# Optimization experiments

Hardware: AMD Instinct MI355X
Metric: run time of the kernel (lower is better)

Reference implementation:

```python
import jax, jax.numpy as jnp
import numpy as np

F, B, D = 32, 8192, 64  # num fields, batch, embedding dim


def setup_inputs() -> dict:
    key = jax.random.key(0)
    inputs = jax.random.normal(key, (F, B, 1, D), dtype=jnp.float32)
    return {"inputs": inputs}


def reference(inputs) -> jnp.ndarray:
    # OPnnLayer with use_reduce=True, use_flatten=True.
    # 1) Add() over the field list -> [B, 1, D]
    s = jnp.sum(inputs, axis=0)  # [B, 1, D]
    # 2) InnerLayer(use_inner=False, perm=[0,2,1]): batch_dot(s^T, s)
    #    [B, D, 1] @ [B, 1, D] -> [B, D, D] (rank-1 outer product per sample)
    outer = jnp.einsum('bod,boe->bde', s, s)  # o == 1
    # 3) Flatten -> [B, D*D]
    return outer.reshape(outer.shape[0], -1)
```

## Files before the change

kernel.cpp:

```cpp
#include <hip/hip_runtime.h>


#define NF 32
#define NB 8192
#define ND 64

__global__ __launch_bounds__(256) void opnn_outer_kernel(
    const float* __restrict__ in, float* __restrict__ out) {
    const int tid = threadIdx.x;
    const int b   = blockIdx.x;
    const int g    = tid >> 4;
    const int dvec = tid & 15;

    const float4* in4 = (const float4*)in;
    size_t i0 = ((size_t)(2 * g)     * NB + b) * (ND / 4) + dvec;
    size_t i1 = ((size_t)(2 * g + 1) * NB + b) * (ND / 4) + dvec;
    float4 a0 = in4[i0];
    float4 a1 = in4[i1];
    float4 acc = make_float4(a0.x + a1.x, a0.y + a1.y, a0.z + a1.z, a0.w + a1.w);

    __shared__ float4 part[16][16];
    __shared__ float4 s4[16];
    part[g][dvec] = acc;
    __syncthreads();

    if (tid < 16) {
        float4 sum = part[0][tid];
        #pragma unroll
        for (int gg = 1; gg < 16; ++gg) {
            float4 p = part[gg][tid];
            sum.x += p.x; sum.y += p.y; sum.z += p.z; sum.w += p.w;
        }
        s4[tid] = sum;
    }
    __syncthreads();

    const float* s = (const float*)s4;
    float4* out4 = (float4*)(out + (size_t)b * (ND * ND));
    #pragma unroll
    for (int j = 0; j < 4; ++j) {
        int idx4 = j * 256 + tid;
        int r  = idx4 >> 4;
        int cv = idx4 & 15;
        float  sr = s[r];
        float4 sc = s4[cv];
        out4[idx4] = make_float4(sr * sc.x, sr * sc.y, sr * sc.z, sr * sc.w);
    }
}

extern "C" void kernel_launch(void* const* d_in, const int* in_sizes, int n_in,
                              void* d_out, int out_size, void* d_ws, size_t ws_size,
                              hipStream_t stream) {
    const float* in = (const float*)d_in[0];
    float* out = (float*)d_out;
    opnn_outer_kernel<<<NB, 256, 0, stream>>>(in, out);
}
```

Measured before the change: 181.6 us.

## Process sixteen samples per block with in-register field sum and nontemporal stores

Each block now handles 16 batch samples instead of one. Each thread sums all 32 fields for its float4 slice in registers, which removes the two-stage shared-memory reduction and one barrier. Each wavefront then writes four samples' outer products using nontemporal loads and stores to keep streaming data out of the cache. The grid shrinks to 512 blocks, which may leave the GPU's compute units less evenly occupied, and the 32 loads per thread are serialized per lane.

```diff
diff --git a/kernel.cpp b/kernel.cpp
--- a/kernel.cpp
+++ b/kernel.cpp
@@ -5,46 +5,45 @@
 #define NB 8192
 #define ND 64
 
+typedef float f4 __attribute__((ext_vector_type(4)));
+
 __global__ __launch_bounds__(256) void opnn_outer_kernel(
     const float* __restrict__ in, float* __restrict__ out) {
-    const int tid = threadIdx.x;
-    const int b   = blockIdx.x;
-    const int g    = tid >> 4;
-    const int dvec = tid & 15;
+    const int tid  = threadIdx.x;
+    const int w    = tid >> 6;
+    const int lane = tid & 63;
+    const int lb   = lane >> 4;
+    const int dv   = lane & 15;
+    const int s_local = w * 4 + lb;
+    const int b = blockIdx.x * 16 + s_local;
 
-    const float4* in4 = (const float4*)in;
-    size_t i0 = ((size_t)(2 * g)     * NB + b) * (ND / 4) + dvec;
-    size_t i1 = ((size_t)(2 * g + 1) * NB + b) * (ND / 4) + dvec;
-    float4 a0 = in4[i0];
-    float4 a1 = in4[i1];
-    float4 acc = make_float4(a0.x + a1.x, a0.y + a1.y, a0.z + a1.z, a0.w + a1.w);
+    const f4* __restrict__ in4 = (const f4*)in;
+    const size_t base = (size_t)b * (ND / 4) + dv;
+    f4 acc = (f4)0.f;
+    #pragma unroll
+    for (int f = 0; f < NF; ++f) {
+        f4 v = __builtin_nontemporal_load(&in4[base + (size_t)f * NB * (ND / 4)]);
+        acc += v;
+    }
 
-    __shared__ float4 part[16][16];
-    __shared__ float4 s4[16];
-    part[g][dvec] = acc;
+    __shared__ f4 sh[16][16];
+    sh[s_local][dv] = acc;
     __syncthreads();
 
-    if (tid < 16) {
-        float4 sum = part[0][tid];
+    const float* shf = (const float*)sh;
+    #pragma unroll
+    for (int ss = 0; ss < 4; ++ss) {
+        const int sidx = w * 4 + ss;
+        const f4 sc = sh[sidx][dv];
+        f4* __restrict__ outp =
+            (f4*)(out + ((size_t)blockIdx.x * 16 + sidx) * (ND * ND));
         #pragma unroll
-        for (int gg = 1; gg < 16; ++gg) {
-            float4 p = part[gg][tid];
-            sum.x += p.x; sum.y += p.y; sum.z += p.z; sum.w += p.w;
+        for (int it = 0; it < 16; ++it) {
+            const int r = it * 4 + lb;
+            const float sr = shf[sidx * 64 + r];
+            f4 v = sr * sc;
+            __builtin_nontemporal_store(v, &outp[it * 64 + lane]);
         }
-        s4[tid] = sum;
-    }
-    __syncthreads();
-
-    const float* s = (const float*)s4;
-    float4* out4 = (float4*)(out + (size_t)b * (ND * ND));
-    #pragma unroll
-    for (int j = 0; j < 4; ++j) {
-        int idx4 = j * 256 + tid;
-        int r  = idx4 >> 4;
-        int cv = idx4 & 15;
-        float  sr = s[r];
-        float4 sc = s4[cv];
-        out4[idx4] = make_float4(sr * sc.x, sr * sc.y, sr * sc.z, sr * sc.w);
     }
 }
 
@@ -53,5 +52,5 @@
                               hipStream_t stream) {
     const float* in = (const float*)d_in[0];
     float* out = (float*)d_out;
-    opnn_outer_kernel<<<NB, 256, 0, stream>>>(in, out);
+    opnn_outer_kernel<<<NB / 16, 256, 0, stream>>>(in, out);
 }
```

Measured after the change: 174.1 us. -4.1%, faster.
